# Performance work log

Hardware: AMD Instinct MI355X
Metric: run time of the kernel (lower is better)

The kernel has to match this reference:

```python
import jax, jax.numpy as jnp
import numpy as np

B, T, D = 8, 2048, 1024
S, W = 512, 16  # num spans, span width


def setup_inputs() -> dict:
    key = jax.random.key(0)
    k1, k2, k3, k4, k5, k6, k7 = jax.random.split(key, 7)
    text_tensor = jax.random.normal(k1, (B, T, D), dtype=jnp.float32)
    contextualized_embedding = jax.random.normal(k2, (B, T, D), dtype=jnp.float32)
    word_indices = jax.random.randint(k3, (B, S, W), 0, T, dtype=jnp.int64)
    word_mask = jax.random.randint(k4, (B, S, W), 0, 2, dtype=jnp.int64)
    word_indices_mask = jax.random.randint(k5, (B, S), 0, 2, dtype=jnp.int64)
    # Linear(input_dim, 1) params
    att_w = jax.random.normal(k6, (D, 1), dtype=jnp.float32) / np.sqrt(D)
    att_b = jax.random.normal(k7, (1,), dtype=jnp.float32) * 0.01
    return {
        "text_tensor": text_tensor,
        "contextualized_embedding": contextualized_embedding,
        "word_indices": word_indices,
        "word_mask": word_mask,
        "word_indices_mask": word_indices_mask,
        "att_w": att_w,
        "att_b": att_b,
    }


def reference(text_tensor, contextualized_embedding, word_indices, word_mask,
              word_indices_mask, att_w, att_b):
    b, t, d = text_tensor.shape
    s, w = word_indices.shape[1], word_indices.shape[2]
    # per-token attention logits: [B, T]
    global_logits = (jnp.einsum("btd,do->bto", text_tensor, att_w) + att_b)[..., 0]
    # relu on indices (clamp negatives to 0), then batched gather
    idx = jnp.maximum(word_indices, 0).astype(jnp.int32)  # [B, S, W]
    flat_idx = idx.reshape(b, s * w)
    # gather span embeddings: [B, S, W, D]
    span_emb = jnp.take_along_axis(text_tensor, flat_idx[:, :, None], axis=1)
    span_emb = span_emb.reshape(b, s, w, d)
    # gather span logits: [B, S, W]
    span_logits = jnp.take_along_axis(global_logits, flat_idx, axis=1).reshape(b, s, w)
    # masked softmax over span width
    mask = word_mask.astype(jnp.bool_)
    masked_logits = jnp.where(mask, span_logits, jnp.float32(-1e9))
    weights = jax.nn.softmax(masked_logits, axis=-1) * mask.astype(span_logits.dtype)
    # weighted sum pooling: [B, S, D]
    attended = jnp.einsum("bswd,bsw->bsd", span_emb, weights)
    return attended * word_indices_mask.astype(attended.dtype)[..., None]
```

## Files before the change

kernel.cpp:

```cpp
#include <hip/hip_runtime.h>

#define NB 8
#define NT 2048
#define ND 1024
#define NS 512
#define NW 16

typedef float f32x4 __attribute__((ext_vector_type(4)));

__global__ __launch_bounds__(256) void span_attn_kernel(
    const float* __restrict__ text,
    const int*   __restrict__ wi,
    const int*   __restrict__ wm,
    const int*   __restrict__ wim,
    const float* __restrict__ att_w,
    const float* __restrict__ att_b,
    float*       __restrict__ out)
{
    const int b    = blockIdx.x & (NB - 1);
    const int wv   = threadIdx.x >> 6;
    const int lane = threadIdx.x & 63;
    const int s    = (blockIdx.x >> 3) * 4 + wv;
    const int bs   = b * NS + s;

    float* orow = out + (size_t)bs * ND + 4 * lane;

    if (wim[bs] == 0) {
        #pragma unroll
        for (int k = 0; k < 4; ++k)
            __builtin_nontemporal_store((f32x4){0.f, 0.f, 0.f, 0.f},
                reinterpret_cast<f32x4*>(orow + 256 * k));
        return;
    }

    const int* wip = wi + (size_t)bs * NW;
    const int* wmp = wm + (size_t)bs * NW;
    int iarr[NW], marr[NW];
    #pragma unroll
    for (int q = 0; q < 4; ++q) {
        const int4 iv = *reinterpret_cast<const int4*>(wip + 4 * q);
        const int4 mv = *reinterpret_cast<const int4*>(wmp + 4 * q);
        iarr[4 * q + 0] = iv.x; iarr[4 * q + 1] = iv.y;
        iarr[4 * q + 2] = iv.z; iarr[4 * q + 3] = iv.w;
        marr[4 * q + 0] = mv.x; marr[4 * q + 1] = mv.y;
        marr[4 * q + 2] = mv.z; marr[4 * q + 3] = mv.w;
    }

    f32x4 wfrag[4];
    #pragma unroll
    for (int k = 0; k < 4; ++k)
        wfrag[k] = *reinterpret_cast<const f32x4*>(att_w + 4 * lane + 256 * k);
    const float bias = att_b[0];

    const float* tbase = text + (size_t)b * NT * ND + 4 * lane;

    f32x4 acc[4];
    #pragma unroll
    for (int k = 0; k < 4; ++k) acc[k] = (f32x4){0.f, 0.f, 0.f, 0.f};
    float esum = 0.0f;

    #pragma unroll
    for (int r = 0; r < NW; ++r) {
        if (marr[r] != 0) {
            const int t = iarr[r] > 0 ? iarr[r] : 0;
            const float* src = tbase + (size_t)t * ND;
            f32x4 f[4];
            #pragma unroll
            for (int k = 0; k < 4; ++k)
                f[k] = *reinterpret_cast<const f32x4*>(src + 256 * k);

            float d = 0.0f;
            #pragma unroll
            for (int k = 0; k < 4; ++k)
                d += f[k].x * wfrag[k].x + f[k].y * wfrag[k].y
                   + f[k].z * wfrag[k].z + f[k].w * wfrag[k].w;
            d += __shfl_xor(d, 1);
            d += __shfl_xor(d, 2);
            d += __shfl_xor(d, 4);
            d += __shfl_xor(d, 8);
            d += __shfl_xor(d, 16);
            d += __shfl_xor(d, 32);

            const float e = __expf(d + bias);
            esum += e;
            #pragma unroll
            for (int k = 0; k < 4; ++k) {
                acc[k].x += e * f[k].x;
                acc[k].y += e * f[k].y;
                acc[k].z += e * f[k].z;
                acc[k].w += e * f[k].w;
            }
        }
    }

    const float inv = esum > 0.0f ? 1.0f / esum : 0.0f;
    #pragma unroll
    for (int k = 0; k < 4; ++k) {
        f32x4 o = acc[k];
        o.x *= inv; o.y *= inv; o.z *= inv; o.w *= inv;
        __builtin_nontemporal_store(o, reinterpret_cast<f32x4*>(orow + 256 * k));
    }
}

extern "C" void kernel_launch(void* const* d_in, const int* in_sizes, int n_in,
                              void* d_out, int out_size, void* d_ws, size_t ws_size,
                              hipStream_t stream) {
    const float* text  = (const float*)d_in[0];
    const int*   wi    = (const int*)d_in[2];
    const int*   wm    = (const int*)d_in[3];
    const int*   wim   = (const int*)d_in[4];
    const float* att_w = (const float*)d_in[5];
    const float* att_b = (const float*)d_in[6];
    float*       out   = (float*)d_out;

    span_attn_kernel<<<dim3(NB * NS / 4), dim3(256), 0, stream>>>(
        text, wi, wm, wim, att_w, att_b, out);
}
```

Before: 16.34 us.

## Use one-wave blocks and iterate set mask bits two rows at a time

Launches one 64-thread block per span instead of four spans per 256-thread block, which removes intra-block wave coupling and gives the scheduler finer-grained work. The span mask is packed into a bitmask and only set bits are visited, two rows per iteration, so the loads of two gathered rows overlap and their shuffle reductions interleave. Indices are read lazily from global memory per row rather than preloaded into registers. The cost is more blocks to launch and a data-dependent loop the compiler cannot fully unroll.

```diff
diff --git a/kernel.cpp b/kernel.cpp
--- a/kernel.cpp
+++ b/kernel.cpp
@@ -8,7 +8,7 @@
 
 typedef float f32x4 __attribute__((ext_vector_type(4)));
 
-__global__ __launch_bounds__(256) void span_attn_kernel(
+__global__ __launch_bounds__(64) void span_attn_kernel(
     const float* __restrict__ text,
     const int*   __restrict__ wi,
     const int*   __restrict__ wm,
@@ -18,10 +18,9 @@
     float*       __restrict__ out)
 {
     const int b    = blockIdx.x & (NB - 1);
-    const int wv   = threadIdx.x >> 6;
-    const int lane = threadIdx.x & 63;
-    const int s    = (blockIdx.x >> 3) * 4 + wv;
+    const int s    = blockIdx.x >> 3;
     const int bs   = b * NS + s;
+    const int lane = threadIdx.x;
 
     float* orow = out + (size_t)bs * ND + 4 * lane;
 
@@ -35,15 +34,15 @@
 
     const int* wip = wi + (size_t)bs * NW;
     const int* wmp = wm + (size_t)bs * NW;
-    int iarr[NW], marr[NW];
+
+    unsigned mkbits = 0;
     #pragma unroll
     for (int q = 0; q < 4; ++q) {
-        const int4 iv = *reinterpret_cast<const int4*>(wip + 4 * q);
         const int4 mv = *reinterpret_cast<const int4*>(wmp + 4 * q);
-        iarr[4 * q + 0] = iv.x; iarr[4 * q + 1] = iv.y;
-        iarr[4 * q + 2] = iv.z; iarr[4 * q + 3] = iv.w;
-        marr[4 * q + 0] = mv.x; marr[4 * q + 1] = mv.y;
-        marr[4 * q + 2] = mv.z; marr[4 * q + 3] = mv.w;
+        mkbits |= (mv.x != 0 ? 1u : 0u) << (4 * q + 0);
+        mkbits |= (mv.y != 0 ? 1u : 0u) << (4 * q + 1);
+        mkbits |= (mv.z != 0 ? 1u : 0u) << (4 * q + 2);
+        mkbits |= (mv.w != 0 ? 1u : 0u) << (4 * q + 3);
     }
 
     f32x4 wfrag[4];
@@ -59,36 +58,68 @@
     for (int k = 0; k < 4; ++k) acc[k] = (f32x4){0.f, 0.f, 0.f, 0.f};
     float esum = 0.0f;
 
-    #pragma unroll
-    for (int r = 0; r < NW; ++r) {
-        if (marr[r] != 0) {
-            const int t = iarr[r] > 0 ? iarr[r] : 0;
-            const float* src = tbase + (size_t)t * ND;
-            f32x4 f[4];
+    unsigned mask = mkbits;
+    while (mask) {
+        const int r0 = __builtin_ctz(mask);
+        mask &= mask - 1;
+        if (mask) {
+            const int r1 = __builtin_ctz(mask);
+            mask &= mask - 1;
+            const int i0 = wip[r0], i1 = wip[r1];
+            const float* s0 = tbase + (size_t)(i0 > 0 ? i0 : 0) * ND;
+            const float* s1 = tbase + (size_t)(i1 > 0 ? i1 : 0) * ND;
+            f32x4 f0[4], f1[4];
+            #pragma unroll
+            for (int k = 0; k < 4; ++k) {
+                f0[k] = *reinterpret_cast<const f32x4*>(s0 + 256 * k);
+                f1[k] = *reinterpret_cast<const f32x4*>(s1 + 256 * k);
+            }
+            float d0 = 0.0f, d1 = 0.0f;
+            #pragma unroll
+            for (int k = 0; k < 4; ++k) {
+                d0 += f0[k].x * wfrag[k].x + f0[k].y * wfrag[k].y
+                    + f0[k].z * wfrag[k].z + f0[k].w * wfrag[k].w;
+                d1 += f1[k].x * wfrag[k].x + f1[k].y * wfrag[k].y
+                    + f1[k].z * wfrag[k].z + f1[k].w * wfrag[k].w;
+            }
+            #pragma unroll
+            for (int sh = 1; sh < 64; sh <<= 1) {
+                d0 += __shfl_xor(d0, sh);
+                d1 += __shfl_xor(d1, sh);
+            }
+            const float e0 = __expf(d0 + bias);
+            const float e1 = __expf(d1 + bias);
+            esum += e0 + e1;
+            #pragma unroll
+            for (int k = 0; k < 4; ++k) {
+                acc[k].x += e0 * f0[k].x + e1 * f1[k].x;
+                acc[k].y += e0 * f0[k].y + e1 * f1[k].y;
+                acc[k].z += e0 * f0[k].z + e1 * f1[k].z;
+                acc[k].w += e0 * f0[k].w + e1 * f1[k].w;
+            }
+        } else {
+            const int i0 = wip[r0];
+            const float* s0 = tbase + (size_t)(i0 > 0 ? i0 : 0) * ND;
+            f32x4 f0[4];
             #pragma unroll
             for (int k = 0; k < 4; ++k)
-                f[k] = *reinterpret_cast<const f32x4*>(src + 256 * k);
-
-            float d = 0.0f;
+                f0[k] = *reinterpret_cast<const f32x4*>(s0 + 256 * k);
+            float d0 = 0.0f;
             #pragma unroll
             for (int k = 0; k < 4; ++k)
-                d += f[k].x * wfrag[k].x + f[k].y * wfrag[k].y
-                   + f[k].z * wfrag[k].z + f[k].w * wfrag[k].w;
-            d += __shfl_xor(d, 1);
-            d += __shfl_xor(d, 2);
-            d += __shfl_xor(d, 4);
-            d += __shfl_xor(d, 8);
-            d += __shfl_xor(d, 16);
-            d += __shfl_xor(d, 32);
-
-            const float e = __expf(d + bias);
-            esum += e;
+                d0 += f0[k].x * wfrag[k].x + f0[k].y * wfrag[k].y
+                    + f0[k].z * wfrag[k].z + f0[k].w * wfrag[k].w;
+            #pragma unroll
+            for (int sh = 1; sh < 64; sh <<= 1)
+                d0 += __shfl_xor(d0, sh);
+            const float e0 = __expf(d0 + bias);
+            esum += e0;
             #pragma unroll
             for (int k = 0; k < 4; ++k) {
-                acc[k].x += e * f[k].x;
-                acc[k].y += e * f[k].y;
-                acc[k].z += e * f[k].z;
-                acc[k].w += e * f[k].w;
+                acc[k].x += e0 * f0[k].x;
+                acc[k].y += e0 * f0[k].y;
+                acc[k].z += e0 * f0[k].z;
+                acc[k].w += e0 * f0[k].w;
             }
         }
     }
@@ -113,6 +144,6 @@
     const float* att_b = (const float*)d_in[6];
     float*       out   = (float*)d_out;
 
-    span_attn_kernel<<<dim3(NB * NS / 4), dim3(256), 0, stream>>>(
+    span_attn_kernel<<<dim3(NB * NS), dim3(64), 0, stream>>>(
         text, wi, wm, wim, att_w, att_b, out);
 }
```

Result: faster. 15.62 us (-4.4%).
